# Performance work log

Measured on AMD Instinct MI355X. Metric: run time of the kernel, lower is better.

Reference implementation:

```python
import jax, jax.numpy as jnp
import numpy as np

B, L, H, N, CIN, COUT, U = 32, 12, 12, 2048, 2, 1, 64
K3 = 3  # num_matrices = n_supports * max_diffusion_step + 1 = 1*2 + 1


def setup_inputs() -> dict:
    rng = np.random.default_rng(0)
    # random sparse-ish symmetric adjacency -> scaled laplacian support (lambda_max ~= 2)
    A = rng.random((N, N), dtype=np.float32)
    A = np.maximum(A, A.T)
    A = A * (A > 0.995)
    d = A.sum(axis=1)
    dis = 1.0 / np.sqrt(np.maximum(d, 1e-6))
    Lap = np.eye(N, dtype=np.float32) - (dis[:, None] * A) * dis[None, :]
    support = (Lap - np.eye(N, dtype=np.float32)).astype(np.float32)  # 2/lmax*L - I with lmax=2

    key = jax.random.key(0)
    ks = jax.random.split(key, 6)

    def w(k, shape, fan):
        return jax.random.normal(k, shape, jnp.float32) / np.float32(np.sqrt(fan))

    Cg_e = (CIN + U) * K3   # 198
    Cg_d = (COUT + U) * K3  # 195
    return {
        "history_data": jax.random.normal(ks[0], (B, L, N, CIN), jnp.float32),
        "support": jnp.asarray(support),
        "enc_Wg": w(ks[1], (Cg_e, 2 * U), Cg_e),
        "enc_bg": jnp.ones((2 * U,), jnp.float32),  # gate bias starts at 1.0 (original repo)
        "enc_Wc": w(ks[2], (Cg_e, U), Cg_e),
        "enc_bc": jnp.zeros((U,), jnp.float32),
        "dec_Wg": w(ks[3], (Cg_d, 2 * U), Cg_d),
        "dec_bg": jnp.ones((2 * U,), jnp.float32),
        "dec_Wc": w(ks[4], (Cg_d, U), Cg_d),
        "dec_bc": jnp.zeros((U,), jnp.float32),
        "Wp": w(ks[5], (U, COUT), U),
        "bp": jnp.zeros((COUT,), jnp.float32),
    }


def _gconv(support, x, W, b):
    # x: [B, N, C]; Chebyshev diffusion T0=x, T1=Sx, T2=2S(Sx)-x, stacked feature-major
    x1 = jnp.einsum('mn,bnc->bmc', support, x)
    x2 = 2.0 * jnp.einsum('mn,bnc->bmc', support, x1) - x
    xs = jnp.stack([x, x1, x2], axis=-1)  # [B, N, C, 3]
    b_, n_, c_, k_ = xs.shape
    y = xs.reshape(b_ * n_, c_ * k_) @ W + b
    return y.reshape(b_, n_, -1)


def _cell(support, x, h, Wg, bg, Wc, bc):
    # DCGRU cell: x [B,N,in], h [B,N,U]
    cat = jnp.concatenate([x, h], axis=-1)
    ru = jax.nn.sigmoid(_gconv(support, cat, Wg, bg))
    r, u = jnp.split(ru, 2, axis=-1)
    c = jnp.tanh(_gconv(support, jnp.concatenate([x, r * h], axis=-1), Wc, bc))
    return u * h + (1.0 - u) * c


def reference(history_data, support, enc_Wg, enc_bg, enc_Wc, enc_bc,
              dec_Wg, dec_bg, dec_Wc, dec_bc, Wp, bp):
    hist = jnp.transpose(history_data, (1, 0, 2, 3))  # [L, B, N, CIN]
    h0 = jnp.zeros((B, N, U), history_data.dtype)

    def enc_step(h, xt):
        return _cell(support, xt, h, enc_Wg, enc_bg, enc_Wc, enc_bc), None

    h_enc, _ = jax.lax.scan(enc_step, h0, hist)

    go = jnp.zeros((B, N, COUT), history_data.dtype)

    def dec_step(carry, _):
        h, xin = carry
        h = _cell(support, xin, h, dec_Wg, dec_bg, dec_Wc, dec_bc)
        out = (h.reshape(-1, U) @ Wp + bp).reshape(B, N, COUT)
        return (h, out), out

    _, outs = jax.lax.scan(dec_step, (h_enc, go), None, length=H)  # [H, B, N, COUT]
    return jnp.transpose(outs, (1, 0, 2, 3))  # [B, H, N, COUT]
```

## Files before the change

kernel.cpp:

```cpp
#include <hip/hip_runtime.h>
#include <math.h>

#define NN 2048
#define BB 32
#define LL 12
#define HHH 12
#define UU 64
#define CE 66
#define WID (BB*CE)
#define MR (NN*BB)
#define SEGW 528
#define CSR_CAP 262144
#define PACK_HALF 28672

typedef short bfrag __attribute__((ext_vector_type(8)));
typedef float ffrag __attribute__((ext_vector_type(4)));

template<int MODE>
__device__ __forceinline__ float vcat_r(const float* __restrict__ inp,
                                        const float* __restrict__ h,
                                        int t, int r, int c) {
  if constexpr (MODE == 1) {
    if (c < 64) return h[(size_t)r*UU + c];
    int q = c - 64;
    int n = r >> 5, b = r & 31;
    return inp[((size_t)(b*LL + t)*NN + n)*2 + q];
  } else {
    if (c < 64) return h[(size_t)r*UU + c];
    if (c == 64) return inp[r];
    return 0.0f;
  }
}

__device__ __forceinline__ float sigm(float x) { return 1.0f / (1.0f + __expf(-x)); }

__device__ __forceinline__ void cvt8(const float* a, bfrag* hi, bfrag* lo) {
  bfrag H, L;
  #pragma unroll
  for (int j = 0; j < 8; ++j) {
    unsigned u = __float_as_uint(a[j]);
    unsigned hb = (u + 0x7FFFu + ((u >> 16) & 1u)) >> 16;
    float rem = a[j] - __uint_as_float(hb << 16);
    unsigned u2 = __float_as_uint(rem);
    unsigned lb = (u2 + 0x7FFFu + ((u2 >> 16) & 1u)) >> 16;
    H[j] = (short)hb; L[j] = (short)lb;
  }
  *hi = H; *lo = L;
}

__global__ __launch_bounds__(256) void k_row_count(const float* __restrict__ S, int* __restrict__ cnt) {
  int m = blockIdx.x;
  const float* row = S + (size_t)m * NN;
  int c = 0;
  for (int i = threadIdx.x; i < NN; i += 256) c += (row[i] != 0.0f);
  __shared__ int sm[4];
  for (int off = 32; off; off >>= 1) c += __shfl_down(c, off, 64);
  if ((threadIdx.x & 63) == 0) sm[threadIdx.x >> 6] = c;
  __syncthreads();
  if (threadIdx.x == 0) cnt[m] = sm[0] + sm[1] + sm[2] + sm[3];
}

__global__ __launch_bounds__(256) void k_scan(const int* __restrict__ cnt, int* __restrict__ rp) {
  __shared__ int tot[256];
  int t = threadIdx.x;
  int base = t * 8;
  int v[8]; int s = 0;
  #pragma unroll
  for (int k = 0; k < 8; ++k) { v[k] = cnt[base + k]; s += v[k]; }
  tot[t] = s;
  __syncthreads();
  for (int off = 1; off < 256; off <<= 1) {
    int add = (t >= off) ? tot[t - off] : 0;
    __syncthreads();
    tot[t] += add;
    __syncthreads();
  }
  int run = (t == 0) ? 0 : tot[t - 1];
  #pragma unroll
  for (int k = 0; k < 8; ++k) { rp[base + k] = run; run += v[k]; }
  if (t == 255) rp[NN] = run;
}

__global__ __launch_bounds__(256) void k_fill(const float* __restrict__ S, const int* __restrict__ rp,
                                              int* __restrict__ cols, float* __restrict__ vals) {
  int m = blockIdx.x;
  const float* row = S + (size_t)m * NN;
  __shared__ int wsum[4];
  __shared__ int chunkbase;
  if (threadIdx.x == 0) chunkbase = rp[m];
  __syncthreads();
  int lane = threadIdx.x & 63, w = threadIdx.x >> 6;
  for (int ch = 0; ch < NN / 256; ++ch) {
    int i = ch * 256 + threadIdx.x;
    float val = row[i];
    bool p = (val != 0.0f);
    unsigned long long mask = __ballot(p);
    int rank = __popcll(mask & ((1ull << lane) - 1ull));
    if (lane == 0) wsum[w] = __popcll(mask);
    __syncthreads();
    int off = 0;
    for (int q = 0; q < w; ++q) off += wsum[q];
    if (p) { int k = chunkbase + off + rank; cols[k] = i; vals[k] = val; }
    __syncthreads();
    if (threadIdx.x == 0) chunkbase += wsum[0] + wsum[1] + wsum[2] + wsum[3];
    __syncthreads();
  }
}

__global__ __launch_bounds__(256) void k_pack(const float* __restrict__ Wsrc, unsigned short* __restrict__ dst,
                                              int CIN_, int NO) {
  int idx = blockIdx.x * 256 + threadIdx.x;
  int nh_count = NO >> 6;
  int tot = nh_count * 7 * 4 * 64 * 8;
  if (idx >= tot) return;
  int j = idx & 7;
  int r1 = idx >> 3;  int lane = r1 & 63;
  int r2 = r1 >> 6;   int nf = r2 & 3;
  int r3 = r2 >> 2;   int ks = r3 % 7; int nh = r3 / 7;
  int grp = lane >> 4, l15 = lane & 15;
  int col = nh*64 + nf*16 + l15;
  float wv = 0.0f;
  if (ks < 6) {
    int kb = ks >> 1;
    int c = CIN_ + (ks & 1)*32 + grp*8 + j;
    wv = Wsrc[((size_t)c*3 + kb)*NO + col];
  } else {
    int q = grp*8 + j;
    if (q < 3*CIN_) { int kb = q / CIN_, c = q % CIN_; wv = Wsrc[((size_t)c*3 + kb)*NO + col]; }
  }
  unsigned u = __float_as_uint(wv);
  unsigned hb = (u + 0x7FFFu + ((u >> 16) & 1u)) >> 16;
  float rem = wv - __uint_as_float(hb << 16);
  unsigned u2 = __float_as_uint(rem);
  unsigned lb = (u2 + 0x7FFFu + ((u2 >> 16) & 1u)) >> 16;
  size_t basehi = ((size_t)nh*PACK_HALF) + ((((size_t)ks*4 + nf)*2 + 0)*64 + lane)*8 + j;
  size_t baselo = ((size_t)nh*PACK_HALF) + ((((size_t)ks*4 + nf)*2 + 1)*64 + lane)*8 + j;
  dst[basehi] = (unsigned short)hb;
  dst[baselo] = (unsigned short)lb;
}

template<int SRC, int X0M>
__global__ __launch_bounds__(256) void k_spmm(
    const int* __restrict__ rp, const int* __restrict__ cols, const float* __restrict__ vals,
    const float* __restrict__ sp, const float* __restrict__ si, const float* __restrict__ sh,
    const float* __restrict__ xp, const float* __restrict__ xi, const float* __restrict__ xh,
    float* __restrict__ Y, int t) {
  __shared__ int   scol[64];
  __shared__ float sval[64];
  int orig = blockIdx.x;
  int swz = (orig & 7) * 1024 + (orig >> 3);
  int seg = swz >> 11;
  int m   = swz & 2047;
  int j0 = rp[m], j1 = rp[m + 1];
  int tid = threadIdx.x;
  float acc0 = 0.f, acc1 = 0.f, acc2 = 0.f;
  int w0 = seg * SEGW + tid, w1 = w0 + 256, w2 = w0 + 512;
  bool a2 = tid < (SEGW - 512);
  int b0 = w0 / CE, c0_ = w0 % CE;
  int b1 = w1 / CE, c1_ = w1 % CE;
  int b2 = w2 / CE, c2_ = w2 % CE;

  auto XV = [&](int n, int w, int b, int c) -> float {
    if constexpr (SRC == 0) return sp[(size_t)n * WID + w];
    else return vcat_r<SRC>(si, sh, t, n * BB + b, c);
  };

  for (int base = j0; base < j1; base += 64) {
    int cnt = min(64, j1 - base);
    if (tid < cnt) { scol[tid] = cols[base + tid]; sval[tid] = vals[base + tid]; }
    __syncthreads();
    int jj = 0;
    for (; jj + 4 <= cnt; jj += 4) {
      int   n0 = scol[jj], n1 = scol[jj+1], n2 = scol[jj+2], n3 = scol[jj+3];
      float s0 = sval[jj], s1 = sval[jj+1], s2 = sval[jj+2], s3 = sval[jj+3];
      float v00 = XV(n0, w0, b0, c0_), v10 = XV(n1, w0, b0, c0_);
      float v20 = XV(n2, w0, b0, c0_), v30 = XV(n3, w0, b0, c0_);
      float v01 = XV(n0, w1, b1, c1_), v11 = XV(n1, w1, b1, c1_);
      float v21 = XV(n2, w1, b1, c1_), v31 = XV(n3, w1, b1, c1_);
      float v02 = 0.f, v12 = 0.f, v22 = 0.f, v32 = 0.f;
      if (a2) {
        v02 = XV(n0, w2, b2, c2_); v12 = XV(n1, w2, b2, c2_);
        v22 = XV(n2, w2, b2, c2_); v32 = XV(n3, w2, b2, c2_);
      }
      acc0 = fmaf(s0, v00, acc0); acc0 = fmaf(s1, v10, acc0);
      acc0 = fmaf(s2, v20, acc0); acc0 = fmaf(s3, v30, acc0);
      acc1 = fmaf(s0, v01, acc1); acc1 = fmaf(s1, v11, acc1);
      acc1 = fmaf(s2, v21, acc1); acc1 = fmaf(s3, v31, acc1);
      acc2 = fmaf(s0, v02, acc2); acc2 = fmaf(s1, v12, acc2);
      acc2 = fmaf(s2, v22, acc2); acc2 = fmaf(s3, v32, acc2);
    }
    for (; jj < cnt; ++jj) {
      int n = scol[jj]; float s = sval[jj];
      acc0 = fmaf(s, XV(n, w0, b0, c0_), acc0);
      acc1 = fmaf(s, XV(n, w1, b1, c1_), acc1);
      if (a2) acc2 = fmaf(s, XV(n, w2, b2, c2_), acc2);
    }
    __syncthreads();
  }

  float* yr = Y + (size_t)m * WID;
  if constexpr (X0M < 0) {
    yr[w0] = acc0; yr[w1] = acc1; if (a2) yr[w2] = acc2;
  } else if constexpr (X0M == 0) {
    const float* x0r = xp + (size_t)m * WID;
    yr[w0] = 2.f * acc0 - x0r[w0];
    yr[w1] = 2.f * acc1 - x0r[w1];
    if (a2) yr[w2] = 2.f * acc2 - x0r[w2];
  } else {
    yr[w0] = 2.f * acc0 - vcat_r<X0M>(xi, xh, t, m * BB + b0, c0_);
    yr[w1] = 2.f * acc1 - vcat_r<X0M>(xi, xh, t, m * BB + b1, c1_);
    if (a2) yr[w2] = 2.f * acc2 - vcat_r<X0M>(xi, xh, t, m * BB + b2, c2_);
  }
}

template<int CATM>
__global__ __launch_bounds__(256, 2) void k_gemm_gate(
    const float* __restrict__ inp, const float* __restrict__ h,
    const float* __restrict__ T1, const float* __restrict__ T2,
    const unsigned short* __restrict__ Bpack, const float* __restrict__ bg,
    float* __restrict__ z, float* __restrict__ Ug, int t) {
  __shared__ unsigned short Bl[PACK_HALF];
  const int CIN_ = (CATM == 1) ? 2 : 1;
  int bid = blockIdx.x;
  int nh = bid & 1;
  int r0 = (bid >> 1) * 128;
  int tid = threadIdx.x;
  {
    const float4* src = (const float4*)(Bpack + (size_t)nh * PACK_HALF);
    float4* dst = (float4*)Bl;
    #pragma unroll
    for (int i = 0; i < 14; ++i) dst[tid + 256*i] = src[tid + 256*i];
  }
  __syncthreads();
  int w = tid >> 6, lane = tid & 63, grp = lane >> 4, l15 = lane & 15;
  int row0 = r0 + w*32 + l15;
  int row1 = row0 + 16;
  ffrag acc[2][4];
  #pragma unroll
  for (int m = 0; m < 2; ++m)
    #pragma unroll
    for (int nf = 0; nf < 4; ++nf) acc[m][nf] = (ffrag){0.f, 0.f, 0.f, 0.f};

  #pragma unroll
  for (int ks = 0; ks < 6; ++ks) {
    int ko = (ks & 1)*32 + grp*8;
    const float* p0 = (ks < 2) ? h : ((ks < 4) ? T1 : T2);
    int st = (ks < 2) ? UU : CE;
    const float* a0p = p0 + (size_t)row0*st + ko;
    const float* a1p = p0 + (size_t)row1*st + ko;
    float av0[8], av1[8];
    *(float4*)(av0)   = *(const float4*)a0p; *(float4*)(av0+4) = *(const float4*)(a0p+4);
    *(float4*)(av1)   = *(const float4*)a1p; *(float4*)(av1+4) = *(const float4*)(a1p+4);
    bfrag ah0, al0, ah1, al1;
    cvt8(av0, &ah0, &al0); cvt8(av1, &ah1, &al1);
    #pragma unroll
    for (int nf = 0; nf < 4; ++nf) {
      bfrag bh  = *(const bfrag*)(Bl + ((((size_t)ks*4 + nf)*2 + 0)*64 + lane)*8);
      bfrag blo = *(const bfrag*)(Bl + ((((size_t)ks*4 + nf)*2 + 1)*64 + lane)*8);
      acc[0][nf] = __builtin_amdgcn_mfma_f32_16x16x32_bf16(ah0, bh,  acc[0][nf], 0, 0, 0);
      acc[0][nf] = __builtin_amdgcn_mfma_f32_16x16x32_bf16(ah0, blo, acc[0][nf], 0, 0, 0);
      acc[0][nf] = __builtin_amdgcn_mfma_f32_16x16x32_bf16(al0, bh,  acc[0][nf], 0, 0, 0);
      acc[1][nf] = __builtin_amdgcn_mfma_f32_16x16x32_bf16(ah1, bh,  acc[1][nf], 0, 0, 0);
      acc[1][nf] = __builtin_amdgcn_mfma_f32_16x16x32_bf16(ah1, blo, acc[1][nf], 0, 0, 0);
      acc[1][nf] = __builtin_amdgcn_mfma_f32_16x16x32_bf16(al1, bh,  acc[1][nf], 0, 0, 0);
    }
  }
  {
    float av0[8] = {0,0,0,0,0,0,0,0}, av1[8] = {0,0,0,0,0,0,0,0};
    if (grp == 0) {
      auto gx = [&](int row, float* av) {
        if (CATM == 1) {
          int n = row >> 5, b = row & 31;
          const float* hp = inp + ((size_t)(b*LL + t)*NN + n)*2;
          av[0] = hp[0]; av[1] = hp[1];
          av[2] = T1[(size_t)row*CE + 64]; av[3] = T1[(size_t)row*CE + 65];
          av[4] = T2[(size_t)row*CE + 64]; av[5] = T2[(size_t)row*CE + 65];
        } else {
          av[0] = inp[row];
          av[1] = T1[(size_t)row*CE + 64];
          av[2] = T2[(size_t)row*CE + 64];
        }
      };
      gx(row0, av0); gx(row1, av1);
    }
    bfrag ah0, al0, ah1, al1;
    cvt8(av0, &ah0, &al0); cvt8(av1, &ah1, &al1);
    #pragma unroll
    for (int nf = 0; nf < 4; ++nf) {
      bfrag bh  = *(const bfrag*)(Bl + ((((size_t)6*4 + nf)*2 + 0)*64 + lane)*8);
      bfrag blo = *(const bfrag*)(Bl + ((((size_t)6*4 + nf)*2 + 1)*64 + lane)*8);
      acc[0][nf] = __builtin_amdgcn_mfma_f32_16x16x32_bf16(ah0, bh,  acc[0][nf], 0, 0, 0);
      acc[0][nf] = __builtin_amdgcn_mfma_f32_16x16x32_bf16(ah0, blo, acc[0][nf], 0, 0, 0);
      acc[0][nf] = __builtin_amdgcn_mfma_f32_16x16x32_bf16(al0, bh,  acc[0][nf], 0, 0, 0);
      acc[1][nf] = __builtin_amdgcn_mfma_f32_16x16x32_bf16(ah1, bh,  acc[1][nf], 0, 0, 0);
      acc[1][nf] = __builtin_amdgcn_mfma_f32_16x16x32_bf16(ah1, blo, acc[1][nf], 0, 0, 0);
      acc[1][nf] = __builtin_amdgcn_mfma_f32_16x16x32_bf16(al1, bh,  acc[1][nf], 0, 0, 0);
    }
  }

  float bgv[4];
  #pragma unroll
  for (int nf = 0; nf < 4; ++nf) bgv[nf] = bg[nh*64 + nf*16 + l15];
  #pragma unroll
  for (int m = 0; m < 2; ++m)
    #pragma unroll
    for (int reg = 0; reg < 4; ++reg) {
      int row = r0 + w*32 + m*16 + grp*4 + reg;
      #pragma unroll
      for (int nf = 0; nf < 4; ++nf) {
        float v = sigm(acc[m][nf][reg] + bgv[nf]);
        int col = nf*16 + l15;
        if (nh == 0) z[(size_t)row*CE + col] = v * h[(size_t)row*UU + col];
        else         Ug[(size_t)row*UU + col] = v;
      }
    }
  if (nh == 0 && l15 == 0) {
    #pragma unroll
    for (int m = 0; m < 2; ++m)
      #pragma unroll
      for (int reg = 0; reg < 4; ++reg) {
        int row = r0 + w*32 + m*16 + grp*4 + reg;
        if (CATM == 1) {
          int n = row >> 5, b = row & 31;
          const float* hp = inp + ((size_t)(b*LL + t)*NN + n)*2;
          z[(size_t)row*CE + 64] = hp[0];
          z[(size_t)row*CE + 65] = hp[1];
        } else {
          z[(size_t)row*CE + 64] = inp[row];
          z[(size_t)row*CE + 65] = 0.0f;
        }
      }
  }
}

template<bool DEC>
__global__ __launch_bounds__(256, 2) void k_gemm_cand(
    const float* __restrict__ z, const float* __restrict__ T1, const float* __restrict__ T2,
    const unsigned short* __restrict__ Bpack, const float* __restrict__ bc,
    const float* __restrict__ Ug, const float* __restrict__ hold,
    float* __restrict__ hnew, const float* __restrict__ Wp, const float* __restrict__ bp,
    float* __restrict__ out, float* __restrict__ xio, int t) {
  __shared__ unsigned short Bl[PACK_HALF];
  const int CIN_ = DEC ? 1 : 2;
  int r0 = blockIdx.x * 128;
  int tid = threadIdx.x;
  {
    const float4* src = (const float4*)Bpack;
    float4* dst = (float4*)Bl;
    #pragma unroll
    for (int i = 0; i < 14; ++i) dst[tid + 256*i] = src[tid + 256*i];
  }
  __syncthreads();
  int w = tid >> 6, lane = tid & 63, grp = lane >> 4, l15 = lane & 15;
  int row0 = r0 + w*32 + l15;
  int row1 = row0 + 16;
  ffrag acc[2][4];
  #pragma unroll
  for (int m = 0; m < 2; ++m)
    #pragma unroll
    for (int nf = 0; nf < 4; ++nf) acc[m][nf] = (ffrag){0.f, 0.f, 0.f, 0.f};

  #pragma unroll
  for (int ks = 0; ks < 6; ++ks) {
    int ko = (ks & 1)*32 + grp*8;
    const float* p0 = (ks < 2) ? z : ((ks < 4) ? T1 : T2);
    const float* a0p = p0 + (size_t)row0*CE + ko;
    const float* a1p = p0 + (size_t)row1*CE + ko;
    float av0[8], av1[8];
    *(float4*)(av0)   = *(const float4*)a0p; *(float4*)(av0+4) = *(const float4*)(a0p+4);
    *(float4*)(av1)   = *(const float4*)a1p; *(float4*)(av1+4) = *(const float4*)(a1p+4);
    bfrag ah0, al0, ah1, al1;
    cvt8(av0, &ah0, &al0); cvt8(av1, &ah1, &al1);
    #pragma unroll
    for (int nf = 0; nf < 4; ++nf) {
      bfrag bh  = *(const bfrag*)(Bl + ((((size_t)ks*4 + nf)*2 + 0)*64 + lane)*8);
      bfrag blo = *(const bfrag*)(Bl + ((((size_t)ks*4 + nf)*2 + 1)*64 + lane)*8);
      acc[0][nf] = __builtin_amdgcn_mfma_f32_16x16x32_bf16(ah0, bh,  acc[0][nf], 0, 0, 0);
      acc[0][nf] = __builtin_amdgcn_mfma_f32_16x16x32_bf16(ah0, blo, acc[0][nf], 0, 0, 0);
      acc[0][nf] = __builtin_amdgcn_mfma_f32_16x16x32_bf16(al0, bh,  acc[0][nf], 0, 0, 0);
      acc[1][nf] = __builtin_amdgcn_mfma_f32_16x16x32_bf16(ah1, bh,  acc[1][nf], 0, 0, 0);
      acc[1][nf] = __builtin_amdgcn_mfma_f32_16x16x32_bf16(ah1, blo, acc[1][nf], 0, 0, 0);
      acc[1][nf] = __builtin_amdgcn_mfma_f32_16x16x32_bf16(al1, bh,  acc[1][nf], 0, 0, 0);
    }
  }
  {
    float av0[8] = {0,0,0,0,0,0,0,0}, av1[8] = {0,0,0,0,0,0,0,0};
    if (grp == 0) {
      auto gx = [&](int row, float* av) {
        #pragma unroll
        for (int q = 0; q < CIN_; ++q) av[q] = z[(size_t)row*CE + 64 + q];
        #pragma unroll
        for (int q = 0; q < CIN_; ++q) av[CIN_ + q] = T1[(size_t)row*CE + 64 + q];
        #pragma unroll
        for (int q = 0; q < CIN_; ++q) av[2*CIN_ + q] = T2[(size_t)row*CE + 64 + q];
      };
      gx(row0, av0); gx(row1, av1);
    }
    bfrag ah0, al0, ah1, al1;
    cvt8(av0, &ah0, &al0); cvt8(av1, &ah1, &al1);
    #pragma unroll
    for (int nf = 0; nf < 4; ++nf) {
      bfrag bh  = *(const bfrag*)(Bl + ((((size_t)6*4 + nf)*2 + 0)*64 + lane)*8);
      bfrag blo = *(const bfrag*)(Bl + ((((size_t)6*4 + nf)*2 + 1)*64 + lane)*8);
      acc[0][nf] = __builtin_amdgcn_mfma_f32_16x16x32_bf16(ah0, bh,  acc[0][nf], 0, 0, 0);
      acc[0][nf] = __builtin_amdgcn_mfma_f32_16x16x32_bf16(ah0, blo, acc[0][nf], 0, 0, 0);
      acc[0][nf] = __builtin_amdgcn_mfma_f32_16x16x32_bf16(al0, bh,  acc[0][nf], 0, 0, 0);
      acc[1][nf] = __builtin_amdgcn_mfma_f32_16x16x32_bf16(ah1, bh,  acc[1][nf], 0, 0, 0);
      acc[1][nf] = __builtin_amdgcn_mfma_f32_16x16x32_bf16(ah1, blo, acc[1][nf], 0, 0, 0);
      acc[1][nf] = __builtin_amdgcn_mfma_f32_16x16x32_bf16(al1, bh,  acc[1][nf], 0, 0, 0);
    }
  }

  float bcv[4], wpv[4];
  #pragma unroll
  for (int nf = 0; nf < 4; ++nf) {
    bcv[nf] = bc[nf*16 + l15];
    wpv[nf] = DEC ? Wp[nf*16 + l15] : 0.f;
  }
  float bp0 = DEC ? bp[0] : 0.f;
  #pragma unroll
  for (int m = 0; m < 2; ++m)
    #pragma unroll
    for (int reg = 0; reg < 4; ++reg) {
      int row = r0 + w*32 + m*16 + grp*4 + reg;
      float p = 0.f;
      #pragma unroll
      for (int nf = 0; nf < 4; ++nf) {
        int col = nf*16 + l15;
        float cf = tanhf(acc[m][nf][reg] + bcv[nf]);
        float u  = Ug[(size_t)row*UU + col];
        float ho = hold[(size_t)row*UU + col];
        float hv = u * ho + (1.0f - u) * cf;
        hnew[(size_t)row*UU + col] = hv;
        if (DEC) p = fmaf(hv, wpv[nf], p);
      }
      if (DEC) {
        p += __shfl_xor(p, 1, 64);
        p += __shfl_xor(p, 2, 64);
        p += __shfl_xor(p, 4, 64);
        p += __shfl_xor(p, 8, 64);
        if (l15 == 0) {
          float val = p + bp0;
          int n = row >> 5, b = row & 31;
          out[((size_t)b*HHH + t)*NN + n] = val;
          xio[row] = val;
        }
      }
    }
}

extern "C" void kernel_launch(void* const* d_in, const int* in_sizes, int n_in,
                              void* d_out, int out_size, void* d_ws, size_t ws_size,
                              hipStream_t stream) {
  (void)in_sizes; (void)n_in; (void)out_size; (void)ws_size;
  const float* hist = (const float*)d_in[0];
  const float* support = (const float*)d_in[1];
  const float* eWg = (const float*)d_in[2];
  const float* ebg = (const float*)d_in[3];
  const float* eWc = (const float*)d_in[4];
  const float* ebc = (const float*)d_in[5];
  const float* dWg = (const float*)d_in[6];
  const float* dbg = (const float*)d_in[7];
  const float* dWc = (const float*)d_in[8];
  const float* dbc = (const float*)d_in[9];
  const float* Wp  = (const float*)d_in[10];
  const float* bp  = (const float*)d_in[11];
  float* out = (float*)d_out;

  char* base = (char*)d_ws;
  size_t off = 0;
  auto carve = [&](size_t bytes) -> void* {
    void* p = base + off;
    off += (bytes + 255) & ~(size_t)255;
    return p;
  };
  int*   cnt   = (int*)carve(NN * 4);
  int*   rpB   = (int*)carve((NN + 1) * 4);
  int*   colsB = (int*)carve(CSR_CAP * 4);
  float* valsB = (float*)carve(CSR_CAP * 4);
  unsigned short* Pge = (unsigned short*)carve(2 * PACK_HALF * 2);
  unsigned short* Pgd = (unsigned short*)carve(2 * PACK_HALF * 2);
  unsigned short* Pce = (unsigned short*)carve((size_t)PACK_HALF * 2);
  unsigned short* Pcd = (unsigned short*)carve((size_t)PACK_HALF * 2);
  float* T1    = (float*)carve((size_t)NN * WID * 4);
  float* T2    = (float*)carve((size_t)NN * WID * 4);
  float* zB    = (float*)carve((size_t)MR * CE * 4);
  float* Ug    = (float*)carve((size_t)MR * UU * 4);
  float* ha    = (float*)carve((size_t)MR * UU * 4);
  float* hb    = (float*)carve((size_t)MR * UU * 4);
  float* xio   = (float*)carve((size_t)MR * 4);

  hipMemsetAsync(ha, 0, (size_t)MR * UU * 4, stream);
  hipMemsetAsync(xio, 0, (size_t)MR * 4, stream);

  k_row_count<<<NN, 256, 0, stream>>>(support, cnt);
  k_scan<<<1, 256, 0, stream>>>(cnt, rpB);
  k_fill<<<NN, 256, 0, stream>>>(support, rpB, colsB, valsB);
  k_pack<<<112, 256, 0, stream>>>(eWg, Pge, 2, 128);
  k_pack<<<56, 256, 0, stream>>>(eWc, Pce, 2, 64);
  k_pack<<<112, 256, 0, stream>>>(dWg, Pgd, 1, 128);
  k_pack<<<56, 256, 0, stream>>>(dWc, Pcd, 1, 64);

  float* hc = ha; float* hn = hb;
  for (int t = 0; t < LL; ++t) {
    k_spmm<1, -1><<<8192, 256, 0, stream>>>(rpB, colsB, valsB, nullptr, hist, hc,
                                            nullptr, nullptr, nullptr, T1, t);
    k_spmm<0, 1><<<8192, 256, 0, stream>>>(rpB, colsB, valsB, T1, nullptr, nullptr,
                                           nullptr, hist, hc, T2, t);
    k_gemm_gate<1><<<MR / 64, 256, 0, stream>>>(hist, hc, T1, T2, Pge, ebg, zB, Ug, t);
    k_spmm<0, -1><<<8192, 256, 0, stream>>>(rpB, colsB, valsB, zB, nullptr, nullptr,
                                            nullptr, nullptr, nullptr, T1, t);
    k_spmm<0, 0><<<8192, 256, 0, stream>>>(rpB, colsB, valsB, T1, nullptr, nullptr,
                                           zB, nullptr, nullptr, T2, t);
    k_gemm_cand<false><<<MR / 128, 256, 0, stream>>>(zB, T1, T2, Pce, ebc, Ug, hc, hn,
                                                     Wp, bp, out, xio, t);
    float* tmp = hc; hc = hn; hn = tmp;
  }
  for (int t = 0; t < HHH; ++t) {
    k_spmm<2, -1><<<8192, 256, 0, stream>>>(rpB, colsB, valsB, nullptr, xio, hc,
                                            nullptr, nullptr, nullptr, T1, t);
    k_spmm<0, 2><<<8192, 256, 0, stream>>>(rpB, colsB, valsB, T1, nullptr, nullptr,
                                           nullptr, xio, hc, T2, t);
    k_gemm_gate<2><<<MR / 64, 256, 0, stream>>>(xio, hc, T1, T2, Pgd, dbg, zB, Ug, t);
    k_spmm<0, -1><<<8192, 256, 0, stream>>>(rpB, colsB, valsB, zB, nullptr, nullptr,
                                            nullptr, nullptr, nullptr, T1, t);
    k_spmm<0, 0><<<8192, 256, 0, stream>>>(rpB, colsB, valsB, T1, nullptr, nullptr,
                                           zB, nullptr, nullptr, T2, t);
    k_gemm_cand<true><<<MR / 128, 256, 0, stream>>>(zB, T1, T2, Pcd, dbc, Ug, hc, hn,
                                                    Wp, bp, out, xio, t);
    float* tmp = hc; hc = hn; hn = tmp;
  }
}
```

Before: 4.593 ms.

## Fuse second diffusion hop into gate/cand GEMMs and store activations as packed bf16 pairs

The second Chebyshev hop (T2 = 2·S·T1 − x) is now computed inside the gate and candidate GEMM kernels. Each block handles four nodes, and T2 stays in shared memory instead of going through a global T2 buffer. All activations (h, T1, z, history, decoder input) are stored as packed hi/lo bf16 words, so the per-GEMM fp32-to-bf16 split conversion goes away and the layout is padded to a stride of 68. tanhf is also replaced by an exp-based fast tanh. The intent is to remove two SpMM launches per step plus their global traffic. The cost is redundant T1 gathers inside the GEMM blocks, the loss of the shared-memory B tile, and slightly lower precision from the truncated low part and fast tanh.

```diff
diff --git a/kernel.cpp b/kernel.cpp
--- a/kernel.cpp
+++ b/kernel.cpp
@@ -6,46 +6,30 @@
 #define LL 12
 #define HHH 12
 #define UU 64
-#define CE 66
-#define WID (BB*CE)
+#define STR 68
+#define SLAB (BB*STR)
+#define SEGP (SLAB/4)
 #define MR (NN*BB)
-#define SEGW 528
 #define CSR_CAP 262144
 #define PACK_HALF 28672
 
 typedef short bfrag __attribute__((ext_vector_type(8)));
 typedef float ffrag __attribute__((ext_vector_type(4)));
 
-template<int MODE>
-__device__ __forceinline__ float vcat_r(const float* __restrict__ inp,
-                                        const float* __restrict__ h,
-                                        int t, int r, int c) {
-  if constexpr (MODE == 1) {
-    if (c < 64) return h[(size_t)r*UU + c];
-    int q = c - 64;
-    int n = r >> 5, b = r & 31;
-    return inp[((size_t)(b*LL + t)*NN + n)*2 + q];
-  } else {
-    if (c < 64) return h[(size_t)r*UU + c];
-    if (c == 64) return inp[r];
-    return 0.0f;
-  }
-}
-
+__device__ __forceinline__ unsigned packsf(float x) {
+  unsigned u = __float_as_uint(x);
+  unsigned hb = (u + 0x7FFFu + ((u >> 16) & 1u)) & 0xFFFF0000u;
+  float rem = x - __uint_as_float(hb);
+  unsigned lb = __float_as_uint(rem) >> 16;
+  return hb | lb;
+}
+__device__ __forceinline__ float recsf(unsigned u) {
+  return __uint_as_float(u & 0xFFFF0000u) + __uint_as_float(u << 16);
+}
 __device__ __forceinline__ float sigm(float x) { return 1.0f / (1.0f + __expf(-x)); }
-
-__device__ __forceinline__ void cvt8(const float* a, bfrag* hi, bfrag* lo) {
-  bfrag H, L;
-  #pragma unroll
-  for (int j = 0; j < 8; ++j) {
-    unsigned u = __float_as_uint(a[j]);
-    unsigned hb = (u + 0x7FFFu + ((u >> 16) & 1u)) >> 16;
-    float rem = a[j] - __uint_as_float(hb << 16);
-    unsigned u2 = __float_as_uint(rem);
-    unsigned lb = (u2 + 0x7FFFu + ((u2 >> 16) & 1u)) >> 16;
-    H[j] = (short)hb; L[j] = (short)lb;
-  }
-  *hi = H; *lo = L;
+__device__ __forceinline__ float tanhfast(float x) {
+  float e = __expf(2.0f * x);
+  return 1.0f - 2.0f / (e + 1.0f);
 }
 
 __global__ __launch_bounds__(256) void k_row_count(const float* __restrict__ S, int* __restrict__ cnt) {
@@ -128,43 +112,54 @@
     int q = grp*8 + j;
     if (q < 3*CIN_) { int kb = q / CIN_, c = q % CIN_; wv = Wsrc[((size_t)c*3 + kb)*NO + col]; }
   }
-  unsigned u = __float_as_uint(wv);
-  unsigned hb = (u + 0x7FFFu + ((u >> 16) & 1u)) >> 16;
-  float rem = wv - __uint_as_float(hb << 16);
-  unsigned u2 = __float_as_uint(rem);
-  unsigned lb = (u2 + 0x7FFFu + ((u2 >> 16) & 1u)) >> 16;
+  unsigned pw = packsf(wv);
   size_t basehi = ((size_t)nh*PACK_HALF) + ((((size_t)ks*4 + nf)*2 + 0)*64 + lane)*8 + j;
   size_t baselo = ((size_t)nh*PACK_HALF) + ((((size_t)ks*4 + nf)*2 + 1)*64 + lane)*8 + j;
-  dst[basehi] = (unsigned short)hb;
-  dst[baselo] = (unsigned short)lb;
-}
-
-template<int SRC, int X0M>
-__global__ __launch_bounds__(256) void k_spmm(
+  dst[basehi] = (unsigned short)(pw >> 16);
+  dst[baselo] = (unsigned short)(pw & 0xFFFFu);
+}
+
+__global__ __launch_bounds__(256) void k_packt(const float* __restrict__ src, unsigned* __restrict__ dst, int n) {
+  int i = blockIdx.x * 256 + threadIdx.x;
+  if (i < n) dst[i] = packsf(src[i]);
+}
+
+template<int SRC>
+__global__ __launch_bounds__(256) void k_hop(
     const int* __restrict__ rp, const int* __restrict__ cols, const float* __restrict__ vals,
-    const float* __restrict__ sp, const float* __restrict__ si, const float* __restrict__ sh,
-    const float* __restrict__ xp, const float* __restrict__ xi, const float* __restrict__ xh,
-    float* __restrict__ Y, int t) {
+    const unsigned* __restrict__ src, const unsigned* __restrict__ xP,
+    const unsigned* __restrict__ hP, unsigned* __restrict__ Y, int t) {
   __shared__ int   scol[64];
   __shared__ float sval[64];
   int orig = blockIdx.x;
   int swz = (orig & 7) * 1024 + (orig >> 3);
   int seg = swz >> 11;
-  int m   = swz & 2047;
-  int j0 = rp[m], j1 = rp[m + 1];
+  int node = swz & 2047;
+  int j0 = rp[node], j1 = rp[node + 1];
   int tid = threadIdx.x;
+  int w0 = seg * SEGP + tid, w1 = w0 + 256, w2 = w0 + 512;
+  bool a2 = tid < (SEGP - 512);
   float acc0 = 0.f, acc1 = 0.f, acc2 = 0.f;
-  int w0 = seg * SEGW + tid, w1 = w0 + 256, w2 = w0 + 512;
-  bool a2 = tid < (SEGW - 512);
-  int b0 = w0 / CE, c0_ = w0 % CE;
-  int b1 = w1 / CE, c1_ = w1 % CE;
-  int b2 = w2 / CE, c2_ = w2 % CE;
-
-  auto XV = [&](int n, int w, int b, int c) -> float {
-    if constexpr (SRC == 0) return sp[(size_t)n * WID + w];
-    else return vcat_r<SRC>(si, sh, t, n * BB + b, c);
+  int b0 = 0, c0 = 0, b1 = 0, c1 = 0, b2 = 0, c2 = 0;
+  if constexpr (SRC != 0) {
+    b0 = w0 / STR; c0 = w0 - b0 * STR;
+    b1 = w1 / STR; c1 = w1 - b1 * STR;
+    b2 = w2 / STR; c2 = w2 - b2 * STR;
+  }
+  auto XV = [&](int n, int wq, int b, int c) -> float {
+    if constexpr (SRC == 0) {
+      return recsf(src[(size_t)n * SLAB + wq]);
+    } else {
+      if (c < 64) return recsf(hP[((size_t)n * BB + b) * UU + c]);
+      if constexpr (SRC == 1) {
+        if (c < 66) return recsf(xP[(((size_t)(b * LL + t)) * NN + n) * 2 + (c - 64)]);
+        return 0.f;
+      } else {
+        if (c == 64) return recsf(xP[(size_t)n * BB + b]);
+        return 0.f;
+      }
+    }
   };
-
   for (int base = j0; base < j1; base += 64) {
     int cnt = min(64, j1 - base);
     if (tid < cnt) { scol[tid] = cols[base + tid]; sval[tid] = vals[base + tid]; }
@@ -173,14 +168,14 @@
     for (; jj + 4 <= cnt; jj += 4) {
       int   n0 = scol[jj], n1 = scol[jj+1], n2 = scol[jj+2], n3 = scol[jj+3];
       float s0 = sval[jj], s1 = sval[jj+1], s2 = sval[jj+2], s3 = sval[jj+3];
-      float v00 = XV(n0, w0, b0, c0_), v10 = XV(n1, w0, b0, c0_);
-      float v20 = XV(n2, w0, b0, c0_), v30 = XV(n3, w0, b0, c0_);
-      float v01 = XV(n0, w1, b1, c1_), v11 = XV(n1, w1, b1, c1_);
-      float v21 = XV(n2, w1, b1, c1_), v31 = XV(n3, w1, b1, c1_);
+      float v00 = XV(n0, w0, b0, c0), v10 = XV(n1, w0, b0, c0);
+      float v20 = XV(n2, w0, b0, c0), v30 = XV(n3, w0, b0, c0);
+      float v01 = XV(n0, w1, b1, c1), v11 = XV(n1, w1, b1, c1);
+      float v21 = XV(n2, w1, b1, c1), v31 = XV(n3, w1, b1, c1);
       float v02 = 0.f, v12 = 0.f, v22 = 0.f, v32 = 0.f;
       if (a2) {
-        v02 = XV(n0, w2, b2, c2_); v12 = XV(n1, w2, b2, c2_);
-        v22 = XV(n2, w2, b2, c2_); v32 = XV(n3, w2, b2, c2_);
+        v02 = XV(n0, w2, b2, c2); v12 = XV(n1, w2, b2, c2);
+        v22 = XV(n2, w2, b2, c2); v32 = XV(n3, w2, b2, c2);
       }
       acc0 = fmaf(s0, v00, acc0); acc0 = fmaf(s1, v10, acc0);
       acc0 = fmaf(s2, v20, acc0); acc0 = fmaf(s3, v30, acc0);
@@ -191,169 +186,260 @@
     }
     for (; jj < cnt; ++jj) {
       int n = scol[jj]; float s = sval[jj];
-      acc0 = fmaf(s, XV(n, w0, b0, c0_), acc0);
-      acc1 = fmaf(s, XV(n, w1, b1, c1_), acc1);
-      if (a2) acc2 = fmaf(s, XV(n, w2, b2, c2_), acc2);
+      acc0 = fmaf(s, XV(n, w0, b0, c0), acc0);
+      acc1 = fmaf(s, XV(n, w1, b1, c1), acc1);
+      if (a2) acc2 = fmaf(s, XV(n, w2, b2, c2), acc2);
     }
     __syncthreads();
   }
-
-  float* yr = Y + (size_t)m * WID;
-  if constexpr (X0M < 0) {
-    yr[w0] = acc0; yr[w1] = acc1; if (a2) yr[w2] = acc2;
-  } else if constexpr (X0M == 0) {
-    const float* x0r = xp + (size_t)m * WID;
-    yr[w0] = 2.f * acc0 - x0r[w0];
-    yr[w1] = 2.f * acc1 - x0r[w1];
-    if (a2) yr[w2] = 2.f * acc2 - x0r[w2];
-  } else {
-    yr[w0] = 2.f * acc0 - vcat_r<X0M>(xi, xh, t, m * BB + b0, c0_);
-    yr[w1] = 2.f * acc1 - vcat_r<X0M>(xi, xh, t, m * BB + b1, c1_);
-    if (a2) yr[w2] = 2.f * acc2 - vcat_r<X0M>(xi, xh, t, m * BB + b2, c2_);
-  }
+  unsigned* yr = Y + (size_t)node * SLAB;
+  yr[w0] = packsf(acc0);
+  yr[w1] = packsf(acc1);
+  if (a2) yr[w2] = packsf(acc2);
 }
 
 template<int CATM>
-__global__ __launch_bounds__(256, 2) void k_gemm_gate(
-    const float* __restrict__ inp, const float* __restrict__ h,
-    const float* __restrict__ T1, const float* __restrict__ T2,
+__global__ __launch_bounds__(256) void k_gate(
+    const unsigned* __restrict__ hP, const unsigned* __restrict__ xP,
+    const unsigned* __restrict__ T1P,
     const unsigned short* __restrict__ Bpack, const float* __restrict__ bg,
-    float* __restrict__ z, float* __restrict__ Ug, int t) {
-  __shared__ unsigned short Bl[PACK_HALF];
-  const int CIN_ = (CATM == 1) ? 2 : 1;
-  int bid = blockIdx.x;
-  int nh = bid & 1;
-  int r0 = (bid >> 1) * 128;
+    const int* __restrict__ rp, const int* __restrict__ cols, const float* __restrict__ vals,
+    unsigned* __restrict__ zP, float* __restrict__ Ug, int t) {
+  __shared__ __align__(16) unsigned short T2hi[4*32*72];
+  __shared__ __align__(16) unsigned short T2lo[4*32*72];
   int tid = threadIdx.x;
-  {
-    const float4* src = (const float4*)(Bpack + (size_t)nh * PACK_HALF);
-    float4* dst = (float4*)Bl;
-    #pragma unroll
-    for (int i = 0; i < 14; ++i) dst[tid + 256*i] = src[tid + 256*i];
+  int nd0 = blockIdx.x * 4;
+  bool k8 = tid < (SLAB - 2048);
+  for (int q = 0; q < 4; ++q) {
+    int node = nd0 + q;
+    int j0 = rp[node], j1 = rp[node + 1];
+    float fa[9];
+    #pragma unroll
+    for (int k = 0; k < 9; ++k) fa[k] = 0.f;
+    int j = j0;
+    for (; j + 2 <= j1; j += 2) {
+      int n0 = cols[j], n1 = cols[j + 1];
+      float s0 = vals[j], s1 = vals[j + 1];
+      const unsigned* p0 = T1P + (size_t)n0 * SLAB + tid;
+      const unsigned* p1 = T1P + (size_t)n1 * SLAB + tid;
+      unsigned u0[9], u1[9];
+      #pragma unroll
+      for (int k = 0; k < 8; ++k) { u0[k] = p0[k*256]; u1[k] = p1[k*256]; }
+      u0[8] = k8 ? p0[2048] : 0u;
+      u1[8] = k8 ? p1[2048] : 0u;
+      #pragma unroll
+      for (int k = 0; k < 9; ++k) {
+        fa[k] = fmaf(s0, recsf(u0[k]), fa[k]);
+        fa[k] = fmaf(s1, recsf(u1[k]), fa[k]);
+      }
+    }
+    if (j < j1) {
+      int n0 = cols[j]; float s0 = vals[j];
+      const unsigned* p0 = T1P + (size_t)n0 * SLAB + tid;
+      unsigned u0[9];
+      #pragma unroll
+      for (int k = 0; k < 8; ++k) u0[k] = p0[k*256];
+      u0[8] = k8 ? p0[2048] : 0u;
+      #pragma unroll
+      for (int k = 0; k < 9; ++k) fa[k] = fmaf(s0, recsf(u0[k]), fa[k]);
+    }
+    #pragma unroll
+    for (int k = 0; k < 9; ++k) {
+      int idx = tid + k*256;
+      if (idx < SLAB) {
+        int b = idx / STR, c = idx - b*STR;
+        int grow = node*BB + b;
+        float x0;
+        if (c < 64) x0 = recsf(hP[(size_t)grow*UU + c]);
+        else if (CATM == 1) x0 = (c < 66) ? recsf(xP[(((size_t)(b*LL + t))*NN + node)*2 + (c - 64)]) : 0.f;
+        else x0 = (c == 64) ? recsf(xP[grow]) : 0.f;
+        unsigned py = packsf(2.f*fa[k] - x0);
+        int sa = (q*32 + b)*72 + c;
+        T2hi[sa] = (unsigned short)(py >> 16);
+        T2lo[sa] = (unsigned short)(py & 0xFFFFu);
+      }
+    }
   }
   __syncthreads();
   int w = tid >> 6, lane = tid & 63, grp = lane >> 4, l15 = lane & 15;
-  int row0 = r0 + w*32 + l15;
-  int row1 = row0 + 16;
-  ffrag acc[2][4];
+  int row0 = nd0*BB + w*32 + l15, row1 = row0 + 16;
+  ffrag acc[2][8];
   #pragma unroll
   for (int m = 0; m < 2; ++m)
     #pragma unroll
-    for (int nf = 0; nf < 4; ++nf) acc[m][nf] = (ffrag){0.f, 0.f, 0.f, 0.f};
-
-  #pragma unroll
-  for (int ks = 0; ks < 6; ++ks) {
+    for (int nf = 0; nf < 8; ++nf) acc[m][nf] = (ffrag){0.f, 0.f, 0.f, 0.f};
+
+  #pragma unroll
+  for (int ks = 0; ks < 7; ++ks) {
     int ko = (ks & 1)*32 + grp*8;
-    const float* p0 = (ks < 2) ? h : ((ks < 4) ? T1 : T2);
-    int st = (ks < 2) ? UU : CE;
-    const float* a0p = p0 + (size_t)row0*st + ko;
-    const float* a1p = p0 + (size_t)row1*st + ko;
-    float av0[8], av1[8];
-    *(float4*)(av0)   = *(const float4*)a0p; *(float4*)(av0+4) = *(const float4*)(a0p+4);
-    *(float4*)(av1)   = *(const float4*)a1p; *(float4*)(av1+4) = *(const float4*)(a1p+4);
     bfrag ah0, al0, ah1, al1;
-    cvt8(av0, &ah0, &al0); cvt8(av1, &ah1, &al1);
-    #pragma unroll
-    for (int nf = 0; nf < 4; ++nf) {
-      bfrag bh  = *(const bfrag*)(Bl + ((((size_t)ks*4 + nf)*2 + 0)*64 + lane)*8);
-      bfrag blo = *(const bfrag*)(Bl + ((((size_t)ks*4 + nf)*2 + 1)*64 + lane)*8);
-      acc[0][nf] = __builtin_amdgcn_mfma_f32_16x16x32_bf16(ah0, bh,  acc[0][nf], 0, 0, 0);
-      acc[0][nf] = __builtin_amdgcn_mfma_f32_16x16x32_bf16(ah0, blo, acc[0][nf], 0, 0, 0);
-      acc[0][nf] = __builtin_amdgcn_mfma_f32_16x16x32_bf16(al0, bh,  acc[0][nf], 0, 0, 0);
-      acc[1][nf] = __builtin_amdgcn_mfma_f32_16x16x32_bf16(ah1, bh,  acc[1][nf], 0, 0, 0);
-      acc[1][nf] = __builtin_amdgcn_mfma_f32_16x16x32_bf16(ah1, blo, acc[1][nf], 0, 0, 0);
-      acc[1][nf] = __builtin_amdgcn_mfma_f32_16x16x32_bf16(al1, bh,  acc[1][nf], 0, 0, 0);
-    }
-  }
-  {
-    float av0[8] = {0,0,0,0,0,0,0,0}, av1[8] = {0,0,0,0,0,0,0,0};
-    if (grp == 0) {
-      auto gx = [&](int row, float* av) {
+    if (ks < 4) {
+      const unsigned* p0 = (ks < 2) ? hP : T1P;
+      int st = (ks < 2) ? UU : STR;
+      const unsigned* a0 = p0 + (size_t)row0*st + ko;
+      const unsigned* a1 = p0 + (size_t)row1*st + ko;
+      uint4 q00 = *(const uint4*)a0, q01 = *(const uint4*)(a0 + 4);
+      uint4 q10 = *(const uint4*)a1, q11 = *(const uint4*)(a1 + 4);
+      unsigned ua0[8] = {q00.x,q00.y,q00.z,q00.w,q01.x,q01.y,q01.z,q01.w};
+      unsigned ua1[8] = {q10.x,q10.y,q10.z,q10.w,q11.x,q11.y,q11.z,q11.w};
+      #pragma unroll
+      for (int jj = 0; jj < 8; ++jj) {
+        ah0[jj] = (short)(ua0[jj] >> 16); al0[jj] = (short)(ua0[jj] & 0xFFFFu);
+        ah1[jj] = (short)(ua1[jj] >> 16); al1[jj] = (short)(ua1[jj] & 0xFFFFu);
+      }
+    } else if (ks < 6) {
+      int sa0 = (w*32 + l15)*72 + ko;
+      int sa1 = (w*32 + l15 + 16)*72 + ko;
+      ah0 = *(const bfrag*)(T2hi + sa0); al0 = *(const bfrag*)(T2lo + sa0);
+      ah1 = *(const bfrag*)(T2hi + sa1); al1 = *(const bfrag*)(T2lo + sa1);
+    } else {
+      unsigned ua0[8] = {0,0,0,0,0,0,0,0}, ua1[8] = {0,0,0,0,0,0,0,0};
+      if (grp == 0) {
+        int sa0 = (w*32 + l15)*72, sa1 = (w*32 + l15 + 16)*72;
+        if (CATM == 1) {
+          int n0r = row0 >> 5, b0r = row0 & 31, b1r = row1 & 31;
+          const unsigned* hx0 = xP + (((size_t)(b0r*LL + t))*NN + n0r)*2;
+          const unsigned* hx1 = xP + (((size_t)(b1r*LL + t))*NN + n0r)*2;
+          ua0[0] = hx0[0]; ua0[1] = hx0[1];
+          ua0[2] = T1P[(size_t)row0*STR + 64]; ua0[3] = T1P[(size_t)row0*STR + 65];
+          ua0[4] = ((unsigned)T2hi[sa0+64] << 16) | T2lo[sa0+64];
+          ua0[5] = ((unsigned)T2hi[sa0+65] << 16) | T2lo[sa0+65];
+          ua1[0] = hx1[0]; ua1[1] = hx1[1];
+          ua1[2] = T1P[(size_t)row1*STR + 64]; ua1[3] = T1P[(size_t)row1*STR + 65];
+          ua1[4] = ((unsigned)T2hi[sa1+64] << 16) | T2lo[sa1+64];
+          ua1[5] = ((unsigned)T2hi[sa1+65] << 16) | T2lo[sa1+65];
+        } else {
+          ua0[0] = xP[row0];
+          ua0[1] = T1P[(size_t)row0*STR + 64];
+          ua0[2] = ((unsigned)T2hi[sa0+64] << 16) | T2lo[sa0+64];
+          ua1[0] = xP[row1];
+          ua1[1] = T1P[(size_t)row1*STR + 64];
+          ua1[2] = ((unsigned)T2hi[sa1+64] << 16) | T2lo[sa1+64];
+        }
+      }
+      #pragma unroll
+      for (int jj = 0; jj < 8; ++jj) {
+        ah0[jj] = (short)(ua0[jj] >> 16); al0[jj] = (short)(ua0[jj] & 0xFFFFu);
+        ah1[jj] = (short)(ua1[jj] >> 16); al1[jj] = (short)(ua1[jj] & 0xFFFFu);
+      }
+    }
+    #pragma unroll
+    for (int nf = 0; nf < 8; ++nf) {
+      const unsigned short* bb = Bpack + (size_t)(nf >> 2)*PACK_HALF
+                               + (((size_t)(ks*4 + (nf & 3))*2)*64 + lane)*8;
+      bfrag bh = *(const bfrag*)bb;
+      bfrag bl = *(const bfrag*)(bb + 512);
+      acc[0][nf] = __builtin_amdgcn_mfma_f32_16x16x32_bf16(ah0, bh, acc[0][nf], 0, 0, 0);
+      acc[0][nf] = __builtin_amdgcn_mfma_f32_16x16x32_bf16(ah0, bl, acc[0][nf], 0, 0, 0);
+      acc[0][nf] = __builtin_amdgcn_mfma_f32_16x16x32_bf16(al0, bh, acc[0][nf], 0, 0, 0);
+      acc[1][nf] = __builtin_amdgcn_mfma_f32_16x16x32_bf16(ah1, bh, acc[1][nf], 0, 0, 0);
+      acc[1][nf] = __builtin_amdgcn_mfma_f32_16x16x32_bf16(ah1, bl, acc[1][nf], 0, 0, 0);
+      acc[1][nf] = __builtin_amdgcn_mfma_f32_16x16x32_bf16(al1, bh, acc[1][nf], 0, 0, 0);
+    }
+  }
+  float bgv[8];
+  #pragma unroll
+  for (int nf = 0; nf < 8; ++nf) bgv[nf] = bg[nf*16 + l15];
+  #pragma unroll
+  for (int m = 0; m < 2; ++m)
+    #pragma unroll
+    for (int reg = 0; reg < 4; ++reg) {
+      int row = nd0*BB + w*32 + m*16 + grp*4 + reg;
+      #pragma unroll
+      for (int nf = 0; nf < 8; ++nf) {
+        int col = nf*16 + l15;
+        float v = sigm(acc[m][nf][reg] + bgv[nf]);
+        if (col < 64) {
+          float ho = recsf(hP[(size_t)row*UU + col]);
+          zP[(size_t)row*STR + col] = packsf(v * ho);
+        } else {
+          Ug[(size_t)row*UU + (col - 64)] = v;
+        }
+      }
+    }
+  if (l15 == 0) {
+    #pragma unroll
+    for (int m = 0; m < 2; ++m)
+      #pragma unroll
+      for (int reg = 0; reg < 4; ++reg) {
+        int row = nd0*BB + w*32 + m*16 + grp*4 + reg;
+        size_t zb = (size_t)row*STR;
         if (CATM == 1) {
           int n = row >> 5, b = row & 31;
-          const float* hp = inp + ((size_t)(b*LL + t)*NN + n)*2;
-          av[0] = hp[0]; av[1] = hp[1];
-          av[2] = T1[(size_t)row*CE + 64]; av[3] = T1[(size_t)row*CE + 65];
-          av[4] = T2[(size_t)row*CE + 64]; av[5] = T2[(size_t)row*CE + 65];
+          const unsigned* hx = xP + (((size_t)(b*LL + t))*NN + n)*2;
+          zP[zb + 64] = hx[0]; zP[zb + 65] = hx[1];
         } else {
-          av[0] = inp[row];
-          av[1] = T1[(size_t)row*CE + 64];
-          av[2] = T2[(size_t)row*CE + 64];
+          zP[zb + 64] = xP[row]; zP[zb + 65] = 0u;
         }
-      };
-      gx(row0, av0); gx(row1, av1);
-    }
-    bfrag ah0, al0, ah1, al1;
-    cvt8(av0, &ah0, &al0); cvt8(av1, &ah1, &al1);
-    #pragma unroll
-    for (int nf = 0; nf < 4; ++nf) {
-      bfrag bh  = *(const bfrag*)(Bl + ((((size_t)6*4 + nf)*2 + 0)*64 + lane)*8);
-      bfrag blo = *(const bfrag*)(Bl + ((((size_t)6*4 + nf)*2 + 1)*64 + lane)*8);
-      acc[0][nf] = __builtin_amdgcn_mfma_f32_16x16x32_bf16(ah0, bh,  acc[0][nf], 0, 0, 0);
-      acc[0][nf] = __builtin_amdgcn_mfma_f32_16x16x32_bf16(ah0, blo, acc[0][nf], 0, 0, 0);
-      acc[0][nf] = __builtin_amdgcn_mfma_f32_16x16x32_bf16(al0, bh,  acc[0][nf], 0, 0, 0);
-      acc[1][nf] = __builtin_amdgcn_mfma_f32_16x16x32_bf16(ah1, bh,  acc[1][nf], 0, 0, 0);
-      acc[1][nf] = __builtin_amdgcn_mfma_f32_16x16x32_bf16(ah1, blo, acc[1][nf], 0, 0, 0);
-      acc[1][nf] = __builtin_amdgcn_mfma_f32_16x16x32_bf16(al1, bh,  acc[1][nf], 0, 0, 0);
-    }
-  }
-
-  float bgv[4];
-  #pragma unroll
-  for (int nf = 0; nf < 4; ++nf) bgv[nf] = bg[nh*64 + nf*16 + l15];
-  #pragma unroll
-  for (int m = 0; m < 2; ++m)
-    #pragma unroll
-    for (int reg = 0; reg < 4; ++reg) {
-      int row = r0 + w*32 + m*16 + grp*4 + reg;
-      #pragma unroll
-      for (int nf = 0; nf < 4; ++nf) {
-        float v = sigm(acc[m][nf][reg] + bgv[nf]);
-        int col = nf*16 + l15;
-        if (nh == 0) z[(size_t)row*CE + col] = v * h[(size_t)row*UU + col];
-        else         Ug[(size_t)row*UU + col] = v;
-      }
-    }
-  if (nh == 0 && l15 == 0) {
-    #pragma unroll
-    for (int m = 0; m < 2; ++m)
-      #pragma unroll
-      for (int reg = 0; reg < 4; ++reg) {
-        int row = r0 + w*32 + m*16 + grp*4 + reg;
-        if (CATM == 1) {
-          int n = row >> 5, b = row & 31;
-          const float* hp = inp + ((size_t)(b*LL + t)*NN + n)*2;
-          z[(size_t)row*CE + 64] = hp[0];
-          z[(size_t)row*CE + 65] = hp[1];
-        } else {
-          z[(size_t)row*CE + 64] = inp[row];
-          z[(size_t)row*CE + 65] = 0.0f;
-        }
+        zP[zb + 66] = 0u; zP[zb + 67] = 0u;
       }
   }
 }
 
 template<bool DEC>
-__global__ __launch_bounds__(256, 2) void k_gemm_cand(
-    const float* __restrict__ z, const float* __restrict__ T1, const float* __restrict__ T2,
+__global__ __launch_bounds__(256) void k_cand(
+    const unsigned* __restrict__ zP, const unsigned* __restrict__ T1P,
     const unsigned short* __restrict__ Bpack, const float* __restrict__ bc,
-    const float* __restrict__ Ug, const float* __restrict__ hold,
-    float* __restrict__ hnew, const float* __restrict__ Wp, const float* __restrict__ bp,
-    float* __restrict__ out, float* __restrict__ xio, int t) {
-  __shared__ unsigned short Bl[PACK_HALF];
+    const float* __restrict__ Ug, const unsigned* __restrict__ hOld,
+    unsigned* __restrict__ hNew,
+    const int* __restrict__ rp, const int* __restrict__ cols, const float* __restrict__ vals,
+    const float* __restrict__ Wp, const float* __restrict__ bp,
+    float* __restrict__ out, unsigned* __restrict__ xioP, int t) {
+  __shared__ __align__(16) unsigned short T2hi[4*32*72];
+  __shared__ __align__(16) unsigned short T2lo[4*32*72];
   const int CIN_ = DEC ? 1 : 2;
-  int r0 = blockIdx.x * 128;
   int tid = threadIdx.x;
-  {
-    const float4* src = (const float4*)Bpack;
-    float4* dst = (float4*)Bl;
-    #pragma unroll
-    for (int i = 0; i < 14; ++i) dst[tid + 256*i] = src[tid + 256*i];
+  int nd0 = blockIdx.x * 4;
+  bool k8 = tid < (SLAB - 2048);
+  for (int q = 0; q < 4; ++q) {
+    int node = nd0 + q;
+    int j0 = rp[node], j1 = rp[node + 1];
+    float fa[9];
+    #pragma unroll
+    for (int k = 0; k < 9; ++k) fa[k] = 0.f;
+    int j = j0;
+    for (; j + 2 <= j1; j += 2) {
+      int n0 = cols[j], n1 = cols[j + 1];
+      float s0 = vals[j], s1 = vals[j + 1];
+      const unsigned* p0 = T1P + (size_t)n0 * SLAB + tid;
+      const unsigned* p1 = T1P + (size_t)n1 * SLAB + tid;
+      unsigned u0[9], u1[9];
+      #pragma unroll
+      for (int k = 0; k < 8; ++k) { u0[k] = p0[k*256]; u1[k] = p1[k*256]; }
+      u0[8] = k8 ? p0[2048] : 0u;
+      u1[8] = k8 ? p1[2048] : 0u;
+      #pragma unroll
+      for (int k = 0; k < 9; ++k) {
+        fa[k] = fmaf(s0, recsf(u0[k]), fa[k]);
+        fa[k] = fmaf(s1, recsf(u1[k]), fa[k]);
+      }
+    }
+    if (j < j1) {
+      int n0 = cols[j]; float s0 = vals[j];
+      const unsigned* p0 = T1P + (size_t)n0 * SLAB + tid;
+      unsigned u0[9];
+      #pragma unroll
+      for (int k = 0; k < 8; ++k) u0[k] = p0[k*256];
+      u0[8] = k8 ? p0[2048] : 0u;
+      #pragma unroll
+      for (int k = 0; k < 9; ++k) fa[k] = fmaf(s0, recsf(u0[k]), fa[k]);
+    }
+    #pragma unroll
+    for (int k = 0; k < 9; ++k) {
+      int idx = tid + k*256;
+      if (idx < SLAB) {
+        float x0 = recsf(zP[(size_t)node*SLAB + idx]);
+        unsigned py = packsf(2.f*fa[k] - x0);
+        int b = idx / STR, c = idx - b*STR;
+        int sa = (q*32 + b)*72 + c;
+        T2hi[sa] = (unsigned short)(py >> 16);
+        T2lo[sa] = (unsigned short)(py & 0xFFFFu);
+      }
+    }
   }
   __syncthreads();
   int w = tid >> 6, lane = tid & 63, grp = lane >> 4, l15 = lane & 15;
-  int row0 = r0 + w*32 + l15;
-  int row1 = row0 + 16;
+  int row0 = nd0*BB + w*32 + l15, row1 = row0 + 16;
   ffrag acc[2][4];
   #pragma unroll
   for (int m = 0; m < 2; ++m)
@@ -361,56 +447,68 @@
     for (int nf = 0; nf < 4; ++nf) acc[m][nf] = (ffrag){0.f, 0.f, 0.f, 0.f};
 
   #pragma unroll
-  for (int ks = 0; ks < 6; ++ks) {
+  for (int ks = 0; ks < 7; ++ks) {
     int ko = (ks & 1)*32 + grp*8;
-    const float* p0 = (ks < 2) ? z : ((ks < 4) ? T1 : T2);
-    const float* a0p = p0 + (size_t)row0*CE + ko;
-    const float* a1p = p0 + (size_t)row1*CE + ko;
-    float av0[8], av1[8];
-    *(float4*)(av0)   = *(const float4*)a0p; *(float4*)(av0+4) = *(const float4*)(a0p+4);
-    *(float4*)(av1)   = *(const float4*)a1p; *(float4*)(av1+4) = *(const float4*)(a1p+4);
     bfrag ah0, al0, ah1, al1;
-    cvt8(av0, &ah0, &al0); cvt8(av1, &ah1, &al1);
+    if (ks < 4) {
+      const unsigned* p0 = (ks < 2) ? zP : T1P;
+      const unsigned* a0 = p0 + (size_t)row0*STR + ko;
+      const unsigned* a1 = p0 + (size_t)row1*STR + ko;
+      uint4 q00 = *(const uint4*)a0, q01 = *(const uint4*)(a0 + 4);
+      uint4 q10 = *(const uint4*)a1, q11 = *(const uint4*)(a1 + 4);
+      unsigned ua0[8] = {q00.x,q00.y,q00.z,q00.w,q01.x,q01.y,q01.z,q01.w};
+      unsigned ua1[8] = {q10.x,q10.y,q10.z,q10.w,q11.x,q11.y,q11.z,q11.w};
+      #pragma unroll
+      for (int jj = 0; jj < 8; ++jj) {
+        ah0[jj] = (short)(ua0[jj] >> 16); al0[jj] = (short)(ua0[jj] & 0xFFFFu);
+        ah1[jj] = (short)(ua1[jj] >> 16); al1[jj] = (short)(ua1[jj] & 0xFFFFu);
+      }
+    } else if (ks < 6) {
+      int sa0 = (w*32 + l15)*72 + ko;
+      int sa1 = (w*32 + l15 + 16)*72 + ko;
+      ah0 = *(const bfrag*)(T2hi + sa0); al0 = *(const bfrag*)(T2lo + sa0);
+      ah1 = *(const bfrag*)(T2hi + sa1); al1 = *(const bfrag*)(T2lo + sa1);
+    } else {
+      unsigned ua0[8] = {0,0,0,0,0,0,0,0}, ua1[8] = {0,0,0,0,0,0,0,0};
+      if (grp == 0) {
+        int sa0 = (w*32 + l15)*72, sa1 = (w*32 + l15 + 16)*72;
+        if (!DEC) {
+          ua0[0] = zP[(size_t)row0*STR + 64];  ua0[1] = zP[(size_t)row0*STR + 65];
+          ua0[2] = T1P[(size_t)row0*STR + 64]; ua0[3] = T1P[(size_t)row0*STR + 65];
+          ua0[4] = ((unsigned)T2hi[sa0+64] << 16) | T2lo[sa0+64];
+          ua0[5] = ((unsigned)T2hi[sa0+65] << 16) | T2lo[sa0+65];
+          ua1[0] = zP[(size_t)row1*STR + 64];  ua1[1] = zP[(size_t)row1*STR + 65];
+          ua1[2] = T1P[(size_t)row1*STR + 64]; ua1[3] = T1P[(size_t)row1*STR + 65];
+          ua1[4] = ((unsigned)T2hi[sa1+64] << 16) | T2lo[sa1+64];
+          ua1[5] = ((unsigned)T2hi[sa1+65] << 16) | T2lo[sa1+65];
+        } else {
+          ua0[0] = zP[(size_t)row0*STR + 64];
+          ua0[1] = T1P[(size_t)row0*STR + 64];
+          ua0[2] = ((unsigned)T2hi[sa0+64] << 16) | T2lo[sa0+64];
+          ua1[0] = zP[(size_t)row1*STR + 64];
+          ua1[1] = T1P[(size_t)row1*STR + 64];
+          ua1[2] = ((unsigned)T2hi[sa1+64] << 16) | T2lo[sa1+64];
+        }
+      }
+      #pragma unroll
+      for (int jj = 0; jj < 8; ++jj) {
+        ah0[jj] = (short)(ua0[jj] >> 16); al0[jj] = (short)(ua0[jj] & 0xFFFFu);
+        ah1[jj] = (short)(ua1[jj] >> 16); al1[jj] = (short)(ua1[jj] & 0xFFFFu);
+      }
+    }
     #pragma unroll
     for (int nf = 0; nf < 4; ++nf) {
-      bfrag bh  = *(const bfrag*)(Bl + ((((size_t)ks*4 + nf)*2 + 0)*64 + lane)*8);
-      bfrag blo = *(const bfrag*)(Bl + ((((size_t)ks*4 + nf)*2 + 1)*64 + lane)*8);
-      acc[0][nf] = __builtin_amdgcn_mfma_f32_16x16x32_bf16(ah0, bh,  acc[0][nf], 0, 0, 0);
-      acc[0][nf] = __builtin_amdgcn_mfma_f32_16x16x32_bf16(ah0, blo, acc[0][nf], 0, 0, 0);
-      acc[0][nf] = __builtin_amdgcn_mfma_f32_16x16x32_bf16(al0, bh,  acc[0][nf], 0, 0, 0);
-      acc[1][nf] = __builtin_amdgcn_mfma_f32_16x16x32_bf16(ah1, bh,  acc[1][nf], 0, 0, 0);
-      acc[1][nf] = __builtin_amdgcn_mfma_f32_16x16x32_bf16(ah1, blo, acc[1][nf], 0, 0, 0);
-      acc[1][nf] = __builtin_amdgcn_mfma_f32_16x16x32_bf16(al1, bh,  acc[1][nf], 0, 0, 0);
-    }
-  }
-  {
-    float av0[8] = {0,0,0,0,0,0,0,0}, av1[8] = {0,0,0,0,0,0,0,0};
-    if (grp == 0) {
-      auto gx = [&](int row, float* av) {
-        #pragma unroll
-        for (int q = 0; q < CIN_; ++q) av[q] = z[(size_t)row*CE + 64 + q];
-        #pragma unroll
-        for (int q = 0; q < CIN_; ++q) av[CIN_ + q] = T1[(size_t)row*CE + 64 + q];
-        #pragma unroll
-        for (int q = 0; q < CIN_; ++q) av[2*CIN_ + q] = T2[(size_t)row*CE + 64 + q];
-      };
-      gx(row0, av0); gx(row1, av1);
-    }
-    bfrag ah0, al0, ah1, al1;
-    cvt8(av0, &ah0, &al0); cvt8(av1, &ah1, &al1);
-    #pragma unroll
-    for (int nf = 0; nf < 4; ++nf) {
-      bfrag bh  = *(const bfrag*)(Bl + ((((size_t)6*4 + nf)*2 + 0)*64 + lane)*8);
-      bfrag blo = *(const bfrag*)(Bl + ((((size_t)6*4 + nf)*2 + 1)*64 + lane)*8);
-      acc[0][nf] = __builtin_amdgcn_mfma_f32_16x16x32_bf16(ah0, bh,  acc[0][nf], 0, 0, 0);
-      acc[0][nf] = __builtin_amdgcn_mfma_f32_16x16x32_bf16(ah0, blo, acc[0][nf], 0, 0, 0);
-      acc[0][nf] = __builtin_amdgcn_mfma_f32_16x16x32_bf16(al0, bh,  acc[0][nf], 0, 0, 0);
-      acc[1][nf] = __builtin_amdgcn_mfma_f32_16x16x32_bf16(ah1, bh,  acc[1][nf], 0, 0, 0);
-      acc[1][nf] = __builtin_amdgcn_mfma_f32_16x16x32_bf16(ah1, blo, acc[1][nf], 0, 0, 0);
-      acc[1][nf] = __builtin_amdgcn_mfma_f32_16x16x32_bf16(al1, bh,  acc[1][nf], 0, 0, 0);
-    }
-  }
-
+      const unsigned short* bb = Bpack + (((size_t)(ks*4 + nf)*2)*64 + lane)*8;
+      bfrag bh = *(const bfrag*)bb;
+      bfrag bl = *(const bfrag*)(bb + 512);
+      acc[0][nf] = __builtin_amdgcn_mfma_f32_16x16x32_bf16(ah0, bh, acc[0][nf], 0, 0, 0);
+      acc[0][nf] = __builtin_amdgcn_mfma_f32_16x16x32_bf16(ah0, bl, acc[0][nf], 0, 0, 0);
+      acc[0][nf] = __builtin_amdgcn_mfma_f32_16x16x32_bf16(al0, bh, acc[0][nf], 0, 0, 0);
+      acc[1][nf] = __builtin_amdgcn_mfma_f32_16x16x32_bf16(ah1, bh, acc[1][nf], 0, 0, 0);
+      acc[1][nf] = __builtin_amdgcn_mfma_f32_16x16x32_bf16(ah1, bl, acc[1][nf], 0, 0, 0);
+      acc[1][nf] = __builtin_amdgcn_mfma_f32_16x16x32_bf16(al1, bh, acc[1][nf], 0, 0, 0);
+    }
+  }
   float bcv[4], wpv[4];
   #pragma unroll
   for (int nf = 0; nf < 4; ++nf) {
@@ -422,16 +520,16 @@
   for (int m = 0; m < 2; ++m)
     #pragma unroll
     for (int reg = 0; reg < 4; ++reg) {
-      int row = r0 + w*32 + m*16 + grp*4 + reg;
+      int row = nd0*BB + w*32 + m*16 + grp*4 + reg;
       float p = 0.f;
       #pragma unroll
       for (int nf = 0; nf < 4; ++nf) {
         int col = nf*16 + l15;
-        float cf = tanhf(acc[m][nf][reg] + bcv[nf]);
+        float cf = tanhfast(acc[m][nf][reg] + bcv[nf]);
         float u  = Ug[(size_t)row*UU + col];
-        float ho = hold[(size_t)row*UU + col];
+        float ho = recsf(hOld[(size_t)row*UU + col]);
         float hv = u * ho + (1.0f - u) * cf;
-        hnew[(size_t)row*UU + col] = hv;
+        hNew[(size_t)row*UU + col] = packsf(hv);
         if (DEC) p = fmaf(hv, wpv[nf], p);
       }
       if (DEC) {
@@ -443,7 +541,7 @@
           float val = p + bp0;
           int n = row >> 5, b = row & 31;
           out[((size_t)b*HHH + t)*NN + n] = val;
-          xio[row] = val;
+          xioP[row] = packsf(val);
         }
       }
     }
@@ -482,16 +580,16 @@
   unsigned short* Pgd = (unsigned short*)carve(2 * PACK_HALF * 2);
   unsigned short* Pce = (unsigned short*)carve((size_t)PACK_HALF * 2);
   unsigned short* Pcd = (unsigned short*)carve((size_t)PACK_HALF * 2);
-  float* T1    = (float*)carve((size_t)NN * WID * 4);
-  float* T2    = (float*)carve((size_t)NN * WID * 4);
-  float* zB    = (float*)carve((size_t)MR * CE * 4);
-  float* Ug    = (float*)carve((size_t)MR * UU * 4);
-  float* ha    = (float*)carve((size_t)MR * UU * 4);
-  float* hb    = (float*)carve((size_t)MR * UU * 4);
-  float* xio   = (float*)carve((size_t)MR * 4);
-
-  hipMemsetAsync(ha, 0, (size_t)MR * UU * 4, stream);
-  hipMemsetAsync(xio, 0, (size_t)MR * 4, stream);
+  unsigned* histP = (unsigned*)carve((size_t)BB * LL * NN * 2 * 4);
+  unsigned* T1P   = (unsigned*)carve((size_t)NN * SLAB * 4);
+  unsigned* zP    = (unsigned*)carve((size_t)NN * SLAB * 4);
+  float*    UgF   = (float*)carve((size_t)MR * UU * 4);
+  unsigned* hPa   = (unsigned*)carve((size_t)MR * UU * 4);
+  unsigned* hPb   = (unsigned*)carve((size_t)MR * UU * 4);
+  unsigned* xioP  = (unsigned*)carve((size_t)MR * 4);
+
+  hipMemsetAsync(hPa, 0, (size_t)MR * UU * 4, stream);
+  hipMemsetAsync(xioP, 0, (size_t)MR * 4, stream);
 
   k_row_count<<<NN, 256, 0, stream>>>(support, cnt);
   k_scan<<<1, 256, 0, stream>>>(cnt, rpB);
@@ -500,34 +598,23 @@
   k_pack<<<56, 256, 0, stream>>>(eWc, Pce, 2, 64);
   k_pack<<<112, 256, 0, stream>>>(dWg, Pgd, 1, 128);
   k_pack<<<56, 256, 0, stream>>>(dWc, Pcd, 1, 64);
-
-  float* hc = ha; float* hn = hb;
+  k_packt<<<(BB*LL*NN*2 + 255)/256, 256, 0, stream>>>(hist, histP, BB*LL*NN*2);
+
+  unsigned* hc = hPa; unsigned* hn = hPb;
   for (int t = 0; t < LL; ++t) {
-    k_spmm<1, -1><<<8192, 256, 0, stream>>>(rpB, colsB, valsB, nullptr, hist, hc,
-                                            nullptr, nullptr, nullptr, T1, t);
-    k_spmm<0, 1><<<8192, 256, 0, stream>>>(rpB, colsB, valsB, T1, nullptr, nullptr,
-                                           nullptr, hist, hc, T2, t);
-    k_gemm_gate<1><<<MR / 64, 256, 0, stream>>>(hist, hc, T1, T2, Pge, ebg, zB, Ug, t);
-    k_spmm<0, -1><<<8192, 256, 0, stream>>>(rpB, colsB, valsB, zB, nullptr, nullptr,
-                                            nullptr, nullptr, nullptr, T1, t);
-    k_spmm<0, 0><<<8192, 256, 0, stream>>>(rpB, colsB, valsB, T1, nullptr, nullptr,
-                                           zB, nullptr, nullptr, T2, t);
-    k_gemm_cand<false><<<MR / 128, 256, 0, stream>>>(zB, T1, T2, Pce, ebc, Ug, hc, hn,
-                                                     Wp, bp, out, xio, t);
-    float* tmp = hc; hc = hn; hn = tmp;
+    k_hop<1><<<8192, 256, 0, stream>>>(rpB, colsB, valsB, nullptr, histP, hc, T1P, t);
+    k_gate<1><<<NN/4, 256, 0, stream>>>(hc, histP, T1P, Pge, ebg, rpB, colsB, valsB, zP, UgF, t);
+    k_hop<0><<<8192, 256, 0, stream>>>(rpB, colsB, valsB, zP, nullptr, nullptr, T1P, t);
+    k_cand<false><<<NN/4, 256, 0, stream>>>(zP, T1P, Pce, ebc, UgF, hc, hn,
+                                            rpB, colsB, valsB, Wp, bp, out, xioP, t);
+    unsigned* tmp = hc; hc = hn; hn = tmp;
   }
   for (int t = 0; t < HHH; ++t) {
-    k_spmm<2, -1><<<8192, 256, 0, stream>>>(rpB, colsB, valsB, nullptr, xio, hc,
-                                            nullptr, nullptr, nullptr, T1, t);
-    k_spmm<0, 2><<<8192, 256, 0, stream>>>(rpB, colsB, valsB, T1, nullptr, nullptr,
-                                           nullptr, xio, hc, T2, t);
-    k_gemm_gate<2><<<MR / 64, 256, 0, stream>>>(xio, hc, T1, T2, Pgd, dbg, zB, Ug, t);
-    k_spmm<0, -1><<<8192, 256, 0, stream>>>(rpB, colsB, valsB, zB, nullptr, nullptr,
-                                            nullptr, nullptr, nullptr, T1, t);
-    k_spmm<0, 0><<<8192, 256, 0, stream>>>(rpB, colsB, valsB, T1, nullptr, nullptr,
-                                           zB, nullptr, nullptr, T2, t);
-    k_gemm_cand<true><<<MR / 128, 256, 0, stream>>>(zB, T1, T2, Pcd, dbc, Ug, hc, hn,
-                                                    Wp, bp, out, xio, t);
-    float* tmp = hc; hc = hn; hn = tmp;
-  }
-}
+    k_hop<2><<<8192, 256, 0, stream>>>(rpB, colsB, valsB, nullptr, xioP, hc, T1P, t);
+    k_gate<2><<<NN/4, 256, 0, stream>>>(hc, xioP, T1P, Pgd, dbg, rpB, colsB, valsB, zP, UgF, t);
+    k_hop<0><<<8192, 256, 0, stream>>>(rpB, colsB, valsB, zP, nullptr, nullptr, T1P, t);
+    k_cand<true><<<NN/4, 256, 0, stream>>>(zP, T1P, Pcd, dbc, UgF, hc, hn,
+                                           rpB, colsB, valsB, Wp, bp, out, xioP, t);
+    unsigned* tmp = hc; hc = hn; hn = tmp;
+  }
+}
```

Measured after the change: 6.670 ms. +45.2%, slower.
